# Kernel tuning notes

Measured on AMD Instinct MI355X. Metric: run time of the kernel, lower is better.

Reference implementation:

```python
import jax, jax.numpy as jnp
import numpy as np

N_NODES = 100000
N_EDGES = 1600000
N_GRAPHS = 64
EMB_DIM = 64
DIMS = [6, 16, 32, 64, EMB_DIM]


def setup_inputs() -> dict:
    key = jax.random.key(0)
    ks = jax.random.split(key, 16)
    feat = jax.random.normal(ks[0], (N_NODES, DIMS[0]), dtype=jnp.float32)
    src = jax.random.randint(ks[1], (N_EDGES,), 0, N_NODES)
    dst = jax.random.randint(ks[2], (N_EDGES,), 0, N_NODES)
    graph_ids = jnp.sort(jax.random.randint(ks[3], (N_NODES,), 0, N_GRAPHS))
    inp = {"feat": feat, "src": src, "dst": dst, "graph_ids": graph_ids}
    # fc_neigh weights for each SAGEConv (gcn aggregator has no fc_self), Xavier-ish init
    for i in range(4):
        din, dout = DIMS[i], DIMS[i + 1]
        scale = 1.0 / np.sqrt(din)
        inp[f"W{i+1}"] = jax.random.uniform(ks[4 + 2 * i], (din, dout), jnp.float32, -scale, scale)
        inp[f"b{i+1}"] = jnp.zeros((dout,), jnp.float32)
    return inp


def _sage_gcn(feat, src, dst, deg, W, b):
    # DGL SAGEConv aggregator_type='gcn':
    # h_neigh = (sum_{u in N(v)} h_u + h_v) / (in_deg(v) + 1); out = h_neigh @ W + b
    neigh = jax.ops.segment_sum(feat[src], dst, num_segments=N_NODES)  # [N, din]
    h = (neigh + feat) / (deg[:, None] + 1.0)
    return h @ W + b


def reference(feat, src, dst, graph_ids, W1, b1, W2, b2, W3, b3, W4, b4):
    deg = jax.ops.segment_sum(jnp.ones((N_EDGES,), feat.dtype), dst, num_segments=N_NODES)
    h = feat
    for W, b in ((W1, b1), (W2, b2), (W3, b3), (W4, b4)):
        h = jax.nn.relu(_sage_gcn(h, src, dst, deg, W, b))
    # dgl.mean_nodes: per-graph mean over nodes
    sums = jax.ops.segment_sum(h, graph_ids, num_segments=N_GRAPHS)          # [G, emb]
    cnts = jax.ops.segment_sum(jnp.ones((N_NODES,), h.dtype), graph_ids, num_segments=N_GRAPHS)
    return sums / jnp.maximum(cnts, 1.0)[:, None]
```

## Files before the change

kernel.cpp:

```cpp
#include <hip/hip_runtime.h>
#include <hip/hip_bf16.h>

#define N_NODES 100000
#define N_EDGES 1600000
#define N_GRAPHS 64

#define NB_BKT 256
#define NPBKT 391
#define EPB 1024
#define NBLK_BIN ((N_EDGES + EPB - 1) / EPB)


__device__ __forceinline__ unsigned int f2bf(float f) {
    unsigned int u = __float_as_uint(f);
    return (u + 0x7fffu + ((u >> 16) & 1u)) >> 16;
}
__device__ __forceinline__ float bf_lo(unsigned int w) { return __uint_as_float(w << 16); }
__device__ __forceinline__ float bf_hi(unsigned int w) { return __uint_as_float(w & 0xffff0000u); }


__global__ __launch_bounds__(256) void bin_count(const int* __restrict__ dst,
                                                 int* __restrict__ cntmat, int E) {
    __shared__ int cnt[NB_BKT];
    int t = threadIdx.x;
    int e0 = blockIdx.x * EPB;
    cnt[t] = 0;
    __syncthreads();
#pragma unroll
    for (int k = 0; k < 4; ++k) {
        int e = e0 + k * 256 + t;
        if (e < E) {
            unsigned d = (unsigned)dst[e];
            atomicAdd(&cnt[d / (unsigned)NPBKT], 1);
        }
    }
    __syncthreads();
    cntmat[(size_t)blockIdx.x * NB_BKT + t] = cnt[t];
}

__global__ __launch_bounds__(256) void bin_scan(int* __restrict__ cntmat,
                                                int* __restrict__ gcnt, int nblk) {
    __shared__ int s[256];
    int b = blockIdx.x, t = threadIdx.x;
    int running = 0;
    for (int c0 = 0; c0 < nblk; c0 += 256) {
        int idx = c0 + t;
        int v = (idx < nblk) ? cntmat[(size_t)idx * NB_BKT + b] : 0;
        s[t] = v;
        __syncthreads();
        for (int o = 1; o < 256; o <<= 1) {
            int a = (t >= o) ? s[t - o] : 0;
            __syncthreads();
            s[t] += a;
            __syncthreads();
        }
        if (idx < nblk) cntmat[(size_t)idx * NB_BKT + b] = running + s[t] - v;
        running += s[255];
        __syncthreads();
    }
    if (t == 0) gcnt[b] = running;
}

__global__ void scan256k(const int* __restrict__ gcnt, int* __restrict__ colbase) {
    __shared__ int s[256];
    int t = threadIdx.x;
    int c = gcnt[t];
    s[t] = c;
    __syncthreads();
    for (int o = 1; o < 256; o <<= 1) {
        int a = (t >= o) ? s[t - o] : 0;
        __syncthreads();
        s[t] += a;
        __syncthreads();
    }
    colbase[t] = s[t] - c;
    if (t == 255) colbase[256] = s[255];
}

__global__ __launch_bounds__(256) void bin_write(const int* __restrict__ dst,
                                                 const int* __restrict__ src,
                                                 const int* __restrict__ cntmat,
                                                 const int* __restrict__ colbase,
                                                 uint2* __restrict__ rec, int E) {
    __shared__ int cnt[NB_BKT];
    __shared__ int lbase[NB_BKT];
    __shared__ int gofs[NB_BKT];
    __shared__ uint2 stage[EPB];
    int t = threadIdx.x;
    int e0 = blockIdx.x * EPB;
    cnt[t] = 0;
    gofs[t] = colbase[t] + cntmat[(size_t)blockIdx.x * NB_BKT + t];
    __syncthreads();
    int myb[4], mypos[4];
    unsigned myd[4], mys[4];
#pragma unroll
    for (int k = 0; k < 4; ++k) {
        int e = e0 + k * 256 + t;
        if (e < E) {
            unsigned d = (unsigned)dst[e];
            int b = (int)(d / (unsigned)NPBKT);
            myd[k] = d;
            mys[k] = (unsigned)src[e];
            myb[k] = b;
            mypos[k] = atomicAdd(&cnt[b], 1);
        } else {
            myb[k] = -1;
        }
    }
    __syncthreads();
    int c = cnt[t];
    lbase[t] = c;
    __syncthreads();
    for (int o = 1; o < 256; o <<= 1) {
        int a = (t >= o) ? lbase[t - o] : 0;
        __syncthreads();
        lbase[t] += a;
        __syncthreads();
    }
    lbase[t] = lbase[t] - c;
    __syncthreads();
#pragma unroll
    for (int k = 0; k < 4; ++k)
        if (myb[k] >= 0) stage[lbase[myb[k]] + mypos[k]] = make_uint2(myd[k], mys[k]);
    __syncthreads();
    int total = min(EPB, E - e0);
    for (int i = t; i < total; i += 256) {
        int lo = 0, hi = NB_BKT - 1;
        while (lo < hi) {
            int m = (lo + hi + 1) >> 1;
            if (lbase[m] <= i) lo = m; else hi = m - 1;
        }
        rec[(size_t)gofs[lo] + (i - lbase[lo])] = stage[i];
    }
}

__global__ __launch_bounds__(256) void fill_bucket(const uint2* __restrict__ rec,
                                                   const int* __restrict__ colbase,
                                                   int* __restrict__ rp,
                                                   int* __restrict__ col, int n) {
    __shared__ int sdeg[512];
    __shared__ int lcur[512];
    __shared__ int lcol[8192];
    int p = blockIdx.x, t = threadIdx.x;
    int nbase = p * NPBKT;
    int nn = min(NPBKT, n - nbase);
    int cbase = colbase[p];
    int cnt = colbase[p + 1] - cbase;
    sdeg[t] = 0;
    sdeg[t + 256] = 0;
    __syncthreads();
    const uint2* r = rec + cbase;
    for (int i = t; i < cnt; i += 256) atomicAdd(&sdeg[r[i].x - (unsigned)nbase], 1);
    __syncthreads();
    int c0 = sdeg[t], c1 = sdeg[t + 256];
    for (int o = 1; o < 512; o <<= 1) {
        int a = (t >= o) ? sdeg[t - o] : 0;
        int b = (t + 256 >= o) ? sdeg[t + 256 - o] : 0;
        __syncthreads();
        sdeg[t] += a;
        sdeg[t + 256] += b;
        __syncthreads();
    }
    int ex0 = sdeg[t] - c0, ex1 = sdeg[t + 256] - c1;
    lcur[t] = ex0;
    lcur[t + 256] = ex1;
    if (t < nn) rp[nbase + t] = cbase + ex0;
    if (t + 256 < nn) rp[nbase + t + 256] = cbase + ex1;
    if (p == NB_BKT - 1 && t == 0) rp[n] = cbase + cnt;
    __syncthreads();
    for (int i = t; i < cnt; i += 256) {
        uint2 e = r[i];
        int slot = atomicAdd(&lcur[e.x - (unsigned)nbase], 1);
        lcol[slot] = (int)e.y;
    }
    __syncthreads();
    for (int i = t; i < cnt; i += 256) col[cbase + i] = lcol[i];
}


__global__ __launch_bounds__(256) void sage_layer1(const float* __restrict__ feat,
                                                   const int* __restrict__ rp,
                                                   const int* __restrict__ col,
                                                   const float* __restrict__ W,
                                                   const float* __restrict__ bias,
                                                   unsigned int* __restrict__ hout, int n) {
    __shared__ float sW[6 * 16];
    __shared__ float sB[16];
    int tid = threadIdx.x;
    if (tid < 96) sW[tid] = W[tid];
    if (tid < 16) sB[tid] = bias[tid];
    __syncthreads();
    int v = blockIdx.x * 256 + tid;
    if (v >= n) return;
    int r0 = rp[v], r1 = rp[v + 1];
    float acc[6] = {0.f, 0.f, 0.f, 0.f, 0.f, 0.f};
    const float2* f2 = reinterpret_cast<const float2*>(feat);
    int j = r0;
    for (; j + 4 <= r1; j += 4) {
        int u0 = col[j], u1 = col[j + 1], u2 = col[j + 2], u3 = col[j + 3];
        float2 a0 = f2[u0 * 3 + 0], b0 = f2[u0 * 3 + 1], c0 = f2[u0 * 3 + 2];
        float2 a1 = f2[u1 * 3 + 0], b1 = f2[u1 * 3 + 1], c1 = f2[u1 * 3 + 2];
        float2 a2 = f2[u2 * 3 + 0], b2 = f2[u2 * 3 + 1], c2 = f2[u2 * 3 + 2];
        float2 a3 = f2[u3 * 3 + 0], b3 = f2[u3 * 3 + 1], c3 = f2[u3 * 3 + 2];
        acc[0] += (a0.x + a1.x) + (a2.x + a3.x);
        acc[1] += (a0.y + a1.y) + (a2.y + a3.y);
        acc[2] += (b0.x + b1.x) + (b2.x + b3.x);
        acc[3] += (b0.y + b1.y) + (b2.y + b3.y);
        acc[4] += (c0.x + c1.x) + (c2.x + c3.x);
        acc[5] += (c0.y + c1.y) + (c2.y + c3.y);
    }
    for (; j < r1; ++j) {
        int u = col[j];
        float2 a = f2[u * 3 + 0], b = f2[u * 3 + 1], c = f2[u * 3 + 2];
        acc[0] += a.x; acc[1] += a.y;
        acc[2] += b.x; acc[3] += b.y;
        acc[4] += c.x; acc[5] += c.y;
    }
    {
        float2 a = f2[v * 3 + 0], b = f2[v * 3 + 1], c = f2[v * 3 + 2];
        acc[0] += a.x; acc[1] += a.y;
        acc[2] += b.x; acc[3] += b.y;
        acc[4] += c.x; acc[5] += c.y;
    }
    float inv = 1.0f / (float)(r1 - r0 + 1);
#pragma unroll
    for (int k = 0; k < 6; ++k) acc[k] *= inv;
    float outv[16];
#pragma unroll
    for (int o = 0; o < 16; ++o) outv[o] = sB[o];
#pragma unroll
    for (int k = 0; k < 6; ++k) {
#pragma unroll
        for (int o = 0; o < 16; ++o) outv[o] += acc[k] * sW[k * 16 + o];
    }
    unsigned int w[8];
#pragma unroll
    for (int o = 0; o < 16; o += 2) {
        unsigned int l = f2bf(fmaxf(outv[o], 0.f));
        unsigned int h = f2bf(fmaxf(outv[o + 1], 0.f));
        w[o / 2] = l | (h << 16);
    }
    uint4* op = reinterpret_cast<uint4*>(hout + (size_t)v * 8);
    op[0] = make_uint4(w[0], w[1], w[2], w[3]);
    op[1] = make_uint4(w[4], w[5], w[6], w[7]);
}


template <int DIN, int DOUT, bool INBF, bool OUTBF>
__global__ __launch_bounds__(256) void sage_u(const void* __restrict__ hin_v,
                                              const int* __restrict__ rp,
                                              const int* __restrict__ col,
                                              const float* __restrict__ W,
                                              const float* __restrict__ bias,
                                              void* __restrict__ hout_v, int n) {
    constexpr int WPN = DIN / 4;
    constexpr int NPB = 256 / WPN;
    constexpr int OPT = DOUT / WPN;
    __shared__ float sW[DIN * DOUT];
    __shared__ float sB[DOUT];
    __shared__ float sH[NPB][DIN + 1];

    int tid = threadIdx.x;
    for (int i = tid; i < DIN * DOUT; i += 256) sW[i] = W[i];
    if (tid < DOUT) sB[tid] = bias[tid];

    int sub = tid / WPN;
    int t = tid % WPN;
    int v = blockIdx.x * NPB + sub;

    const float4* hin4 = reinterpret_cast<const float4*>(hin_v);
    const uint2* hin2 = reinterpret_cast<const uint2*>(hin_v);

    auto load4 = [&](int u) -> float4 {
        if constexpr (INBF) {
            uint2 w = hin2[(size_t)u * (DIN / 4) + t];
            float4 r;
            r.x = bf_lo(w.x); r.y = bf_hi(w.x);
            r.z = bf_lo(w.y); r.w = bf_hi(w.y);
            return r;
        } else {
            return hin4[(size_t)u * (DIN / 4) + t];
        }
    };

    if (v < n) {
        int r0 = rp[v], r1 = rp[v + 1];
        float4 a0 = {0.f, 0.f, 0.f, 0.f}, a1 = {0.f, 0.f, 0.f, 0.f};
        float4 a2 = {0.f, 0.f, 0.f, 0.f}, a3 = {0.f, 0.f, 0.f, 0.f};
        int j = r0;
        for (; j + 4 <= r1; j += 4) {
            int u0 = col[j], u1 = col[j + 1], u2 = col[j + 2], u3 = col[j + 3];
            float4 x0 = load4(u0);
            float4 x1 = load4(u1);
            float4 x2 = load4(u2);
            float4 x3 = load4(u3);
            a0.x += x0.x; a0.y += x0.y; a0.z += x0.z; a0.w += x0.w;
            a1.x += x1.x; a1.y += x1.y; a1.z += x1.z; a1.w += x1.w;
            a2.x += x2.x; a2.y += x2.y; a2.z += x2.z; a2.w += x2.w;
            a3.x += x3.x; a3.y += x3.y; a3.z += x3.z; a3.w += x3.w;
        }
        for (; j < r1; ++j) {
            float4 x = load4(col[j]);
            a0.x += x.x; a0.y += x.y; a0.z += x.z; a0.w += x.w;
        }
        float4 sx = load4(v);
        float inv = 1.0f / (float)(r1 - r0 + 1);
        sH[sub][t * 4 + 0] = ((a0.x + a1.x) + (a2.x + a3.x) + sx.x) * inv;
        sH[sub][t * 4 + 1] = ((a0.y + a1.y) + (a2.y + a3.y) + sx.y) * inv;
        sH[sub][t * 4 + 2] = ((a0.z + a1.z) + (a2.z + a3.z) + sx.z) * inv;
        sH[sub][t * 4 + 3] = ((a0.w + a1.w) + (a2.w + a3.w) + sx.w) * inv;
    }
    __syncthreads();
    if (v < n) {
        int o0 = t * OPT;
        float accO[OPT];
#pragma unroll
        for (int i = 0; i < OPT; ++i) accO[i] = sB[o0 + i];
#pragma unroll 4
        for (int k = 0; k < DIN; ++k) {
            float hk = sH[sub][k];
#pragma unroll
            for (int i = 0; i < OPT; ++i) accO[i] += hk * sW[k * DOUT + o0 + i];
        }
        if constexpr (OUTBF) {
            unsigned int w[OPT / 2];
#pragma unroll
            for (int i = 0; i < OPT; i += 2) {
                unsigned int l = f2bf(fmaxf(accO[i], 0.f));
                unsigned int h = f2bf(fmaxf(accO[i + 1], 0.f));
                w[i / 2] = l | (h << 16);
            }
            unsigned int* op = reinterpret_cast<unsigned int*>(hout_v) +
                               (size_t)v * (DOUT / 2) + o0 / 2;
            if constexpr (OPT / 2 == 4) {
                *reinterpret_cast<uint4*>(op) = make_uint4(w[0], w[1], w[2], w[3]);
            } else if constexpr (OPT / 2 == 2) {
                *reinterpret_cast<uint2*>(op) = make_uint2(w[0], w[1]);
            } else {
                *op = w[0];
            }
        } else {
            float* hout = reinterpret_cast<float*>(hout_v);
#pragma unroll
            for (int i = 0; i < OPT; i += 4) {
                float4 rr;
                rr.x = fmaxf(accO[i + 0], 0.f);
                rr.y = fmaxf(accO[i + 1], 0.f);
                rr.z = fmaxf(accO[i + 2], 0.f);
                rr.w = fmaxf(accO[i + 3], 0.f);
                *reinterpret_cast<float4*>(hout + (size_t)v * DOUT + o0 + i) = rr;
            }
        }
    }
}


__device__ __forceinline__ int lower_bound_i(const int* __restrict__ a, int n, int key) {
    int lo = 0, hi = n;
    while (lo < hi) {
        int m = (lo + hi) >> 1;
        if (a[m] < key) lo = m + 1; else hi = m;
    }
    return lo;
}

__global__ __launch_bounds__(256) void pool_bf(const unsigned int* __restrict__ h32,
                                               const int* __restrict__ gids,
                                               float* __restrict__ out, int n) {
    int bx = blockIdx.x;
    int g = bx >> 3, s = bx & 7;
    int start = lower_bound_i(gids, n, g);
    int end = lower_bound_i(gids, n, g + 1);
    int len = end - start;
    float inv = 1.0f / (float)(len > 0 ? len : 1);
    int chunk = (len + 7) / 8;
    int s0 = start + s * chunk;
    int s1 = min(s0 + chunk, end);
    int t = threadIdx.x;
    int d = t & 31, j = t >> 5;
    float a0 = 0.f, a1 = 0.f;
    for (int i = s0 + j; i < s1; i += 8) {
        unsigned int w = h32[(size_t)i * 32 + d];
        a0 += bf_lo(w);
        a1 += bf_hi(w);
    }
    __shared__ float red[8][32][2];
    red[j][d][0] = a0;
    red[j][d][1] = a1;
    __syncthreads();
    if (t < 64) {
        int dd = t & 31, e = t >> 5;
        float tot = 0.f;
#pragma unroll
        for (int k = 0; k < 8; ++k) tot += red[k][dd][e];
        atomicAdd(&out[g * 64 + 2 * dd + e], tot * inv);
    }
}


extern "C" void kernel_launch(void* const* d_in, const int* in_sizes, int n_in,
                              void* d_out, int out_size, void* d_ws, size_t ws_size,
                              hipStream_t stream) {
    const int N = N_NODES, E = N_EDGES;
    const float* feat = (const float*)d_in[0];
    const int* src = (const int*)d_in[1];
    const int* dst = (const int*)d_in[2];
    const int* gids = (const int*)d_in[3];
    const float* W1 = (const float*)d_in[4];
    const float* b1 = (const float*)d_in[5];
    const float* W2 = (const float*)d_in[6];
    const float* b2 = (const float*)d_in[7];
    const float* W3 = (const float*)d_in[8];
    const float* b3 = (const float*)d_in[9];
    const float* W4 = (const float*)d_in[10];
    const float* b4 = (const float*)d_in[11];
    float* out = (float*)d_out;

    int* rp = (int*)d_ws;
    int* gcnt = rp + (N + 1);
    int* colbase = gcnt + 256;
    int* cntmat = colbase + 257;
    int* col = cntmat + (size_t)NBLK_BIN * 256;
    size_t off = (size_t)((char*)(col + E) - (char*)d_ws);
    off = (off + 255) & ~(size_t)255;
    unsigned int* h1 = (unsigned int*)((char*)d_ws + off);
    unsigned int* h2 = h1 + (size_t)N * 8;
    unsigned int* h3 = h2 + (size_t)N * 16;
    unsigned int* h4 = h3 + (size_t)N * 32;
    uint2* rec = (uint2*)h3;

    hipMemsetAsync(out, 0, (size_t)N_GRAPHS * 64 * sizeof(float), stream);

    bin_count<<<NBLK_BIN, 256, 0, stream>>>(dst, cntmat, E);
    bin_scan<<<NB_BKT, 256, 0, stream>>>(cntmat, gcnt, NBLK_BIN);
    scan256k<<<1, 256, 0, stream>>>(gcnt, colbase);
    bin_write<<<NBLK_BIN, 256, 0, stream>>>(dst, src, cntmat, colbase, rec, E);
    fill_bucket<<<NB_BKT, 256, 0, stream>>>(rec, colbase, rp, col, N);

    sage_layer1<<<(N + 255) / 256, 256, 0, stream>>>(feat, rp, col, W1, b1, h1, N);
    sage_u<16, 32, true, true><<<(N + 63) / 64, 256, 0, stream>>>(h1, rp, col, W2, b2, h2, N);
    sage_u<32, 64, true, true><<<(N + 31) / 32, 256, 0, stream>>>(h2, rp, col, W3, b3, h3, N);
    sage_u<64, 64, true, true><<<(N + 15) / 16, 256, 0, stream>>>(h3, rp, col, W4, b4, h4, N);

    pool_bf<<<N_GRAPHS * 8, 256, 0, stream>>>(h4, gids, out, N);
}
```

Baseline: 190.3 us.

## Switch intermediate activations from bf16 to fp16 with packed half2 accumulation

```diff
diff --git a/kernel.cpp b/kernel.cpp
--- a/kernel.cpp
+++ b/kernel.cpp
@@ -1,5 +1,6 @@
 #include <hip/hip_runtime.h>
 #include <hip/hip_bf16.h>
+#include <hip/hip_fp16.h>
 
 #define N_NODES 100000
 #define N_EDGES 1600000
@@ -11,12 +12,15 @@
 #define NBLK_BIN ((N_EDGES + EPB - 1) / EPB)
 
 
-__device__ __forceinline__ unsigned int f2bf(float f) {
-    unsigned int u = __float_as_uint(f);
-    return (u + 0x7fffu + ((u >> 16) & 1u)) >> 16;
-}
-__device__ __forceinline__ float bf_lo(unsigned int w) { return __uint_as_float(w << 16); }
-__device__ __forceinline__ float bf_hi(unsigned int w) { return __uint_as_float(w & 0xffff0000u); }
+__device__ __forceinline__ __half2 u2h(unsigned int u) {
+    return __builtin_bit_cast(__half2, u);
+}
+__device__ __forceinline__ float2 u2f2(unsigned int u) {
+    return __half22float2(u2h(u));
+}
+__device__ __forceinline__ unsigned int packh2(float a, float b) {
+    return __builtin_bit_cast(unsigned int, __float22half2_rn(make_float2(a, b)));
+}
 
 
 __global__ __launch_bounds__(256) void bin_count(const int* __restrict__ dst,
@@ -235,25 +239,22 @@
     }
     unsigned int w[8];
 #pragma unroll
-    for (int o = 0; o < 16; o += 2) {
-        unsigned int l = f2bf(fmaxf(outv[o], 0.f));
-        unsigned int h = f2bf(fmaxf(outv[o + 1], 0.f));
-        w[o / 2] = l | (h << 16);
-    }
-    uint4* op = reinterpret_cast<uint4*>(hout + (size_t)v * 8);
+    for (int o = 0; o < 16; o += 2)
+        w[o / 2] = packh2(fmaxf(outv[o], 0.f), fmaxf(outv[o + 1], 0.f));
+    uint4* op = reinterpret_cast<uint4*>(hout + v * 8);
     op[0] = make_uint4(w[0], w[1], w[2], w[3]);
     op[1] = make_uint4(w[4], w[5], w[6], w[7]);
 }
 
 
-template <int DIN, int DOUT, bool INBF, bool OUTBF>
-__global__ __launch_bounds__(256) void sage_u(const void* __restrict__ hin_v,
-                                              const int* __restrict__ rp,
-                                              const int* __restrict__ col,
-                                              const float* __restrict__ W,
-                                              const float* __restrict__ bias,
-                                              void* __restrict__ hout_v, int n) {
-    constexpr int WPN = DIN / 4;
+template <int DIN, int DOUT>
+__global__ __launch_bounds__(256) void sage_f16(const uint4* __restrict__ hin,
+                                                const int* __restrict__ rp,
+                                                const int* __restrict__ col,
+                                                const float* __restrict__ W,
+                                                const float* __restrict__ bias,
+                                                unsigned int* __restrict__ hout, int n) {
+    constexpr int WPN = DIN / 8;
     constexpr int NPB = 256 / WPN;
     constexpr int OPT = DOUT / WPN;
     __shared__ float sW[DIN * DOUT];
@@ -268,47 +269,45 @@
     int t = tid % WPN;
     int v = blockIdx.x * NPB + sub;
 
-    const float4* hin4 = reinterpret_cast<const float4*>(hin_v);
-    const uint2* hin2 = reinterpret_cast<const uint2*>(hin_v);
-
-    auto load4 = [&](int u) -> float4 {
-        if constexpr (INBF) {
-            uint2 w = hin2[(size_t)u * (DIN / 4) + t];
-            float4 r;
-            r.x = bf_lo(w.x); r.y = bf_hi(w.x);
-            r.z = bf_lo(w.y); r.w = bf_hi(w.y);
-            return r;
-        } else {
-            return hin4[(size_t)u * (DIN / 4) + t];
-        }
-    };
-
     if (v < n) {
         int r0 = rp[v], r1 = rp[v + 1];
-        float4 a0 = {0.f, 0.f, 0.f, 0.f}, a1 = {0.f, 0.f, 0.f, 0.f};
-        float4 a2 = {0.f, 0.f, 0.f, 0.f}, a3 = {0.f, 0.f, 0.f, 0.f};
+        const __half2 z = __float2half2_rn(0.f);
+        __half2 a0[4] = {z, z, z, z}, a1[4] = {z, z, z, z};
+        __half2 a2[4] = {z, z, z, z}, a3[4] = {z, z, z, z};
         int j = r0;
         for (; j + 4 <= r1; j += 4) {
             int u0 = col[j], u1 = col[j + 1], u2 = col[j + 2], u3 = col[j + 3];
-            float4 x0 = load4(u0);
-            float4 x1 = load4(u1);
-            float4 x2 = load4(u2);
-            float4 x3 = load4(u3);
-            a0.x += x0.x; a0.y += x0.y; a0.z += x0.z; a0.w += x0.w;
-            a1.x += x1.x; a1.y += x1.y; a1.z += x1.z; a1.w += x1.w;
-            a2.x += x2.x; a2.y += x2.y; a2.z += x2.z; a2.w += x2.w;
-            a3.x += x3.x; a3.y += x3.y; a3.z += x3.z; a3.w += x3.w;
+            uint4 w0 = hin[u0 * WPN + t];
+            uint4 w1 = hin[u1 * WPN + t];
+            uint4 w2 = hin[u2 * WPN + t];
+            uint4 w3 = hin[u3 * WPN + t];
+            a0[0] = __hadd2(a0[0], u2h(w0.x)); a0[1] = __hadd2(a0[1], u2h(w0.y));
+            a0[2] = __hadd2(a0[2], u2h(w0.z)); a0[3] = __hadd2(a0[3], u2h(w0.w));
+            a1[0] = __hadd2(a1[0], u2h(w1.x)); a1[1] = __hadd2(a1[1], u2h(w1.y));
+            a1[2] = __hadd2(a1[2], u2h(w1.z)); a1[3] = __hadd2(a1[3], u2h(w1.w));
+            a2[0] = __hadd2(a2[0], u2h(w2.x)); a2[1] = __hadd2(a2[1], u2h(w2.y));
+            a2[2] = __hadd2(a2[2], u2h(w2.z)); a2[3] = __hadd2(a2[3], u2h(w2.w));
+            a3[0] = __hadd2(a3[0], u2h(w3.x)); a3[1] = __hadd2(a3[1], u2h(w3.y));
+            a3[2] = __hadd2(a3[2], u2h(w3.z)); a3[3] = __hadd2(a3[3], u2h(w3.w));
         }
         for (; j < r1; ++j) {
-            float4 x = load4(col[j]);
-            a0.x += x.x; a0.y += x.y; a0.z += x.z; a0.w += x.w;
-        }
-        float4 sx = load4(v);
+            uint4 w = hin[col[j] * WPN + t];
+            a0[0] = __hadd2(a0[0], u2h(w.x)); a0[1] = __hadd2(a0[1], u2h(w.y));
+            a0[2] = __hadd2(a0[2], u2h(w.z)); a0[3] = __hadd2(a0[3], u2h(w.w));
+        }
+#pragma unroll
+        for (int q = 0; q < 4; ++q)
+            a0[q] = __hadd2(__hadd2(a0[q], a1[q]), __hadd2(a2[q], a3[q]));
+        uint4 ws = hin[v * WPN + t];
+        unsigned swd[4] = {ws.x, ws.y, ws.z, ws.w};
         float inv = 1.0f / (float)(r1 - r0 + 1);
-        sH[sub][t * 4 + 0] = ((a0.x + a1.x) + (a2.x + a3.x) + sx.x) * inv;
-        sH[sub][t * 4 + 1] = ((a0.y + a1.y) + (a2.y + a3.y) + sx.y) * inv;
-        sH[sub][t * 4 + 2] = ((a0.z + a1.z) + (a2.z + a3.z) + sx.z) * inv;
-        sH[sub][t * 4 + 3] = ((a0.w + a1.w) + (a2.w + a3.w) + sx.w) * inv;
+#pragma unroll
+        for (int q = 0; q < 4; ++q) {
+            float2 f = __half22float2(a0[q]);
+            float2 s = u2f2(swd[q]);
+            sH[sub][t * 8 + 2 * q + 0] = (f.x + s.x) * inv;
+            sH[sub][t * 8 + 2 * q + 1] = (f.y + s.y) * inv;
+        }
     }
     __syncthreads();
     if (v < n) {
@@ -322,34 +321,18 @@
 #pragma unroll
             for (int i = 0; i < OPT; ++i) accO[i] += hk * sW[k * DOUT + o0 + i];
         }
-        if constexpr (OUTBF) {
-            unsigned int w[OPT / 2];
-#pragma unroll
-            for (int i = 0; i < OPT; i += 2) {
-                unsigned int l = f2bf(fmaxf(accO[i], 0.f));
-                unsigned int h = f2bf(fmaxf(accO[i + 1], 0.f));
-                w[i / 2] = l | (h << 16);
-            }
-            unsigned int* op = reinterpret_cast<unsigned int*>(hout_v) +
-                               (size_t)v * (DOUT / 2) + o0 / 2;
-            if constexpr (OPT / 2 == 4) {
-                *reinterpret_cast<uint4*>(op) = make_uint4(w[0], w[1], w[2], w[3]);
-            } else if constexpr (OPT / 2 == 2) {
-                *reinterpret_cast<uint2*>(op) = make_uint2(w[0], w[1]);
-            } else {
-                *op = w[0];
-            }
+        unsigned wds[OPT / 2];
+#pragma unroll
+        for (int i = 0; i < OPT; i += 2)
+            wds[i / 2] = packh2(fmaxf(accO[i], 0.f), fmaxf(accO[i + 1], 0.f));
+        unsigned* op = hout + v * (DOUT / 2) + o0 / 2;
+        if constexpr (OPT / 2 == 4) {
+            *reinterpret_cast<uint4*>(op) = make_uint4(wds[0], wds[1], wds[2], wds[3]);
+        } else if constexpr (OPT / 2 == 8) {
+            reinterpret_cast<uint4*>(op)[0] = make_uint4(wds[0], wds[1], wds[2], wds[3]);
+            reinterpret_cast<uint4*>(op)[1] = make_uint4(wds[4], wds[5], wds[6], wds[7]);
         } else {
-            float* hout = reinterpret_cast<float*>(hout_v);
-#pragma unroll
-            for (int i = 0; i < OPT; i += 4) {
-                float4 rr;
-                rr.x = fmaxf(accO[i + 0], 0.f);
-                rr.y = fmaxf(accO[i + 1], 0.f);
-                rr.z = fmaxf(accO[i + 2], 0.f);
-                rr.w = fmaxf(accO[i + 3], 0.f);
-                *reinterpret_cast<float4*>(hout + (size_t)v * DOUT + o0 + i) = rr;
-            }
+            *reinterpret_cast<uint2*>(op) = make_uint2(wds[0], wds[1]);
         }
     }
 }
@@ -364,9 +347,9 @@
     return lo;
 }
 
-__global__ __launch_bounds__(256) void pool_bf(const unsigned int* __restrict__ h32,
-                                               const int* __restrict__ gids,
-                                               float* __restrict__ out, int n) {
+__global__ __launch_bounds__(256) void pool_f16(const unsigned int* __restrict__ h32,
+                                                const int* __restrict__ gids,
+                                                float* __restrict__ out, int n) {
     int bx = blockIdx.x;
     int g = bx >> 3, s = bx & 7;
     int start = lower_bound_i(gids, n, g);
@@ -380,9 +363,9 @@
     int d = t & 31, j = t >> 5;
     float a0 = 0.f, a1 = 0.f;
     for (int i = s0 + j; i < s1; i += 8) {
-        unsigned int w = h32[(size_t)i * 32 + d];
-        a0 += bf_lo(w);
-        a1 += bf_hi(w);
+        float2 f = u2f2(h32[(size_t)i * 32 + d]);
+        a0 += f.x;
+        a1 += f.y;
     }
     __shared__ float red[8][32][2];
     red[j][d][0] = a0;
@@ -438,9 +421,12 @@
     fill_bucket<<<NB_BKT, 256, 0, stream>>>(rec, colbase, rp, col, N);
 
     sage_layer1<<<(N + 255) / 256, 256, 0, stream>>>(feat, rp, col, W1, b1, h1, N);
-    sage_u<16, 32, true, true><<<(N + 63) / 64, 256, 0, stream>>>(h1, rp, col, W2, b2, h2, N);
-    sage_u<32, 64, true, true><<<(N + 31) / 32, 256, 0, stream>>>(h2, rp, col, W3, b3, h3, N);
-    sage_u<64, 64, true, true><<<(N + 15) / 16, 256, 0, stream>>>(h3, rp, col, W4, b4, h4, N);
-
-    pool_bf<<<N_GRAPHS * 8, 256, 0, stream>>>(h4, gids, out, N);
-}
+    sage_f16<16, 32><<<(N + 127) / 128, 256, 0, stream>>>(
+        (const uint4*)h1, rp, col, W2, b2, h2, N);
+    sage_f16<32, 64><<<(N + 63) / 64, 256, 0, stream>>>(
+        (const uint4*)h2, rp, col, W3, b3, h3, N);
+    sage_f16<64, 64><<<(N + 31) / 32, 256, 0, stream>>>(
+        (const uint4*)h3, rp, col, W4, b4, h4, N);
+
+    pool_f16<<<N_GRAPHS * 8, 256, 0, stream>>>(h4, gids, out, N);
+}
```

Measured after the change: 183.2 us. 3.8% less time.
